# Kernel tuning notes

Measured on AMD Instinct MI355X. Metric: run time of the kernel, lower is better.

Reference implementation:

```python
import jax, jax.numpy as jnp
import numpy as np
from jax import lax

TAGSET_SIZE = 64
START_TAG = TAGSET_SIZE - 2
STOP_TAG = TAGSET_SIZE - 1
NEG_INF = -10000.0


def setup_inputs() -> dict:
    key = jax.random.key(0)
    k_feat, k_trans, k_tags = jax.random.split(key, 3)
    B, S, T = 512, 1024, TAGSET_SIZE
    feats = jax.random.normal(k_feat, (B, S, T), dtype=jnp.float32)
    transitions = jax.random.normal(k_trans, (T, T), dtype=jnp.float32)
    # CRF constraints: nothing transitions FROM anything into START row semantics
    # of the torch code: transitions[START, :] = -1e4 ; transitions[:, STOP] = -1e4
    transitions = transitions.at[START_TAG, :].set(NEG_INF)
    transitions = transitions.at[:, STOP_TAG].set(NEG_INF)
    tags = jax.random.randint(k_tags, (B, S), 0, T - 2, dtype=jnp.int64)
    mask = jnp.ones((B, S), dtype=jnp.int32)
    return {"feats": feats, "transitions": transitions, "tags": tags, "mask": mask}


def _forward_alg(feats, transitions, maskf):
    # feats: (B,S,T), maskf: (B,S) float
    B, S, T = feats.shape
    init = jnp.full((B, T), NEG_INF, dtype=feats.dtype).at[:, START_TAG].set(0.0)

    def step(fv, xs):
        feat, m = xs  # feat: (B,T), m: (B,)
        # next_tag_var[b, next, prev] = fv[b,prev] + trans[next,prev] + feat[b,next]
        nxt = jax.nn.logsumexp(
            fv[:, None, :] + transitions[None, :, :] + feat[:, :, None], axis=2
        )
        m1 = m[:, None]
        return nxt * m1 + fv * (1.0 - m1), None

    fv, _ = lax.scan(step, init, (feats.transpose(1, 0, 2), maskf.T))
    terminal = fv + transitions[STOP_TAG][None, :]
    return jax.nn.logsumexp(terminal, axis=1)  # (B,)


def _score_sentence(feats, transitions, tags, maskf):
    B, S, T = feats.shape
    tags_ext = jnp.concatenate(
        [jnp.full((B, 1), START_TAG, dtype=tags.dtype), tags], axis=1
    )  # (B, S+1)
    cur = tags_ext[:, 1:]   # (B,S)
    prev = tags_ext[:, :-1]  # (B,S)
    emit = jnp.take_along_axis(feats, cur[:, :, None], axis=2)[:, :, 0]  # (B,S)
    trans = transitions[cur, prev]  # (B,S)
    score = jnp.sum((emit + trans) * maskf, axis=1)
    last_idx = maskf.sum(axis=1).astype(jnp.int32)  # index into tags_ext
    last_tags = jnp.take_along_axis(tags_ext, last_idx[:, None].astype(tags.dtype), axis=1)[:, 0]
    return score + transitions[STOP_TAG, last_tags]


def reference(feats, transitions, tags, mask):
    maskf = mask.astype(feats.dtype)
    forward_score = _forward_alg(feats, transitions, maskf)
    gold_score = _score_sentence(feats, transitions, tags, maskf)
    return jnp.mean(forward_score - gold_score)
```

## Files before the change

kernel.cpp:

```cpp
#include <hip/hip_runtime.h>

#define START_TAG 62
#define STOP_TAG 63
#define BATCH 512
#define SLEN 1024
#define NCHAIN 64

typedef float vf4 __attribute__((ext_vector_type(4)));
typedef short short8 __attribute__((ext_vector_type(8)));

#define E_OFF_FLOATS (1u << 18)
#define E_BYTES      134217728ull
#define WS_NEEDED    (1048576ull + E_BYTES + 65536ull)

__device__ __forceinline__ unsigned pk_bf16(float lo, float hi) {
  return __builtin_amdgcn_perm(__float_as_uint(hi), __float_as_uint(lo), 0x07060302u);
}
__device__ __forceinline__ short bf16_rne(float x) {
  unsigned u = __float_as_uint(x);
  u += 0x7FFFu + ((u >> 16) & 1u);
  return (short)(u >> 16);
}
__device__ __forceinline__ vf4 mfma16(short8 a, short8 b, vf4 c) {
  return __builtin_amdgcn_mfma_f32_16x16x32_bf16(a, b, c, 0, 0, 0);
}

template<int DIR>
__device__ __forceinline__ void load_A(const float* __restrict__ trans, short8 A[4][2],
                                       int q, int col) {
  const int mrow = 16 * (col >> 2) + (col & 3);
  #pragma unroll
  for (int t = 0; t < 4; ++t) {
    #pragma unroll
    for (int c = 0; c < 2; ++c) {
      short8 a;
      #pragma unroll
      for (int j = 0; j < 8; ++j) {
        int R = mrow + 4 * t, K = 16 * q + 8 * c + j;
        float tv = (DIR == 0) ? trans[R * 64 + K] : trans[K * 64 + R];
        a[j] = bf16_rne(__expf(tv));
      }
      A[t][c] = a;
    }
  }
}

template<int DIR>
__device__ __forceinline__ void epilogue(float* __restrict__ ws, const float W[16],
                                         float C, int g, int lane, int q, int col) {
  float* slab = ws + (size_t)(g * 2 + DIR) * 1024;
  #pragma unroll
  for (int t4 = 0; t4 < 4; ++t4) {
    vf4 o = {W[t4 * 4], W[t4 * 4 + 1], W[t4 * 4 + 2], W[t4 * 4 + 3]};
    *(vf4*)(slab + lane * 16 + t4 * 4) = o;
  }
  if (q == 0) ws[65536 + (g * 2 + DIR) * 16 + col] = C;
}

template<int DIR>
__device__ __forceinline__ void crf_step(const vf4 (&Fs)[4], const short8 (&A)[4][2],
                                         float (&W)[16]) {
  float P[16];
  #pragma unroll
  for (int t = 0; t < 4; ++t)
    #pragma unroll
    for (int i = 0; i < 4; ++i)
      P[t * 4 + i] = (DIR == 0) ? W[t * 4 + i] : W[t * 4 + i] * Fs[t][i];

  union { unsigned uu[4]; short8 s8; } B0, B1;
  B0.uu[0] = pk_bf16(P[0], P[1]);   B0.uu[1] = pk_bf16(P[2], P[3]);
  B0.uu[2] = pk_bf16(P[4], P[5]);   B0.uu[3] = pk_bf16(P[6], P[7]);
  B1.uu[0] = pk_bf16(P[8], P[9]);   B1.uu[1] = pk_bf16(P[10], P[11]);
  B1.uu[2] = pk_bf16(P[12], P[13]); B1.uu[3] = pk_bf16(P[14], P[15]);

  vf4 z4 = {0.f, 0.f, 0.f, 0.f};
  vf4 d0 = mfma16(A[0][0], B0.s8, z4);
  vf4 d1 = mfma16(A[1][0], B0.s8, z4);
  vf4 d2 = mfma16(A[2][0], B0.s8, z4);
  vf4 d3 = mfma16(A[3][0], B0.s8, z4);
  d0 = mfma16(A[0][1], B1.s8, d0);
  d1 = mfma16(A[1][1], B1.s8, d1);
  d2 = mfma16(A[2][1], B1.s8, d2);
  d3 = mfma16(A[3][1], B1.s8, d3);

  #pragma unroll
  for (int i = 0; i < 4; ++i) {
    W[i]      = (DIR == 0) ? d0[i] * Fs[0][i] : d0[i];
    W[4 + i]  = (DIR == 0) ? d1[i] * Fs[1][i] : d1[i];
    W[8 + i]  = (DIR == 0) ? d2[i] * Fs[2][i] : d2[i];
    W[12 + i] = (DIR == 0) ? d3[i] * Fs[3][i] : d3[i];
  }
}

template<int DIR>
__device__ __forceinline__ void chain_fast_x(const float* E,
                                             const float* __restrict__ trans,
                                             float* __restrict__ ws, int g) {
  const int lane = threadIdx.x & 63;
  const int q = lane >> 4, col = lane & 15;

  short8 A[4][2];
  load_A<DIR>(trans, A, q, col);

  float W[16];
  if (DIR == 0) {
    #pragma unroll
    for (int i = 0; i < 16; ++i) W[i] = 0.f;
    if (q == 3) W[14] = 1.f;
  } else {
    #pragma unroll
    for (int i = 0; i < 16; ++i) W[i] = __expf(trans[STOP_TAG * 64 + 16 * q + i]);
  }

  const vf4* sp = (const vf4*)E + (((size_t)(g * 2 + DIR) * 512) << 8)
                  + (q << 4) + col;

  vf4 F[8][4];
  #pragma unroll
  for (int p = 0; p < 8; ++p)
    #pragma unroll
    for (int k = 0; k < 4; ++k)
      F[p][k] = sp[(size_t)p * 256 + k * 64];

  float C = 0.f, zpend = 1.f;

  for (int bk = 0; bk < 63; ++bk) {
    #pragma unroll
    for (int u = 0; u < 8; ++u) {
      crf_step<DIR>(F[u], A, W);
      const int jn = bk * 8 + u + 8;
      #pragma unroll
      for (int k = 0; k < 4; ++k)
        F[u][k] = sp[(size_t)jn * 256 + k * 64];
      if ((u & 3) == 3) {
        float rz = __builtin_amdgcn_rcpf(zpend);
        C += __logf(zpend);
        #pragma unroll
        for (int i = 0; i < 16; ++i) W[i] *= rz;
        zpend = __shfl(W[0], col);
      }
      __builtin_amdgcn_sched_barrier(0);
    }
  }

  #pragma unroll
  for (int u = 0; u < 8; ++u) {
    crf_step<DIR>(F[u], A, W);
    if ((u & 3) == 3) {
      float rz = __builtin_amdgcn_rcpf(zpend);
      C += __logf(zpend);
      #pragma unroll
      for (int i = 0; i < 16; ++i) W[i] *= rz;
      zpend = __shfl(W[0], col);
    }
  }

  epilogue<DIR>(ws, W, C, g, lane, q, col);
}

template<int DIR>
__device__ __forceinline__ void chain_masked(const float* __restrict__ feats,
                                             const float* __restrict__ trans,
                                             const int* __restrict__ mask,
                                             float* __restrict__ ws, int g) {
  const int lane = threadIdx.x & 63;
  const int q = lane >> 4, col = lane & 15;
  const int b = g * 16 + col;

  short8 A[4][2];
  load_A<DIR>(trans, A, q, col);

  float W[16];
  float C = 0.f;
  if (DIR == 0) {
    #pragma unroll
    for (int i = 0; i < 16; ++i) W[i] = 0.f;
    if (q == 3) W[14] = 1.f;
  } else {
    #pragma unroll
    for (int i = 0; i < 16; ++i) W[i] = __expf(trans[STOP_TAG * 64 + 16 * q + i]);
  }

  const char* gb = (const char*)feats + (size_t)b * 262144 + (size_t)q * 64;
  vf4 cur[4];
  {
    size_t s0 = (DIR == 0) ? 0 : 1023;
    #pragma unroll
    for (int v = 0; v < 4; ++v)
      cur[v] = *(const vf4*)(gb + s0 * 256 + (size_t)v * 16);
  }

  for (int grp = 0; grp < 128; ++grp) {
    #pragma unroll
    for (int u = 0; u < 4; ++u) {
      const int j = grp * 4 + u;
      float e[16];
      #pragma unroll
      for (int v = 0; v < 4; ++v)
        #pragma unroll
        for (int i = 0; i < 4; ++i) e[v * 4 + i] = __expf(cur[v][i]);

      float P[16];
      #pragma unroll
      for (int i = 0; i < 16; ++i) P[i] = (DIR == 0) ? W[i] : W[i] * e[i];

      union { unsigned uu[4]; short8 s8; } B0, B1;
      B0.uu[0] = pk_bf16(P[0], P[1]);   B0.uu[1] = pk_bf16(P[2], P[3]);
      B0.uu[2] = pk_bf16(P[4], P[5]);   B0.uu[3] = pk_bf16(P[6], P[7]);
      B1.uu[0] = pk_bf16(P[8], P[9]);   B1.uu[1] = pk_bf16(P[10], P[11]);
      B1.uu[2] = pk_bf16(P[12], P[13]); B1.uu[3] = pk_bf16(P[14], P[15]);

      vf4 z4 = {0.f, 0.f, 0.f, 0.f};
      vf4 d0 = mfma16(A[0][0], B0.s8, z4);
      vf4 d1 = mfma16(A[1][0], B0.s8, z4);
      vf4 d2 = mfma16(A[2][0], B0.s8, z4);
      vf4 d3 = mfma16(A[3][0], B0.s8, z4);
      d0 = mfma16(A[0][1], B1.s8, d0);
      d1 = mfma16(A[1][1], B1.s8, d1);
      d2 = mfma16(A[2][1], B1.s8, d2);
      d3 = mfma16(A[3][1], B1.s8, d3);

      int sj = (DIR == 0) ? j : 1023 - j;
      int m = mask[b * 1024 + sj];
      int sn = (DIR == 0) ? (j + 1) : 1023 - (j + 1);
      #pragma unroll
      for (int v = 0; v < 4; ++v)
        cur[v] = *(const vf4*)(gb + (size_t)sn * 256 + (size_t)v * 16);

      #pragma unroll
      for (int i = 0; i < 4; ++i) {
        float n0 = (DIR == 0) ? d0[i] * e[i]      : d0[i];
        float n1 = (DIR == 0) ? d1[i] * e[4 + i]  : d1[i];
        float n2 = (DIR == 0) ? d2[i] * e[8 + i]  : d2[i];
        float n3 = (DIR == 0) ? d3[i] * e[12 + i] : d3[i];
        W[i]      = m ? n0 : W[i];
        W[4 + i]  = m ? n1 : W[4 + i];
        W[8 + i]  = m ? n2 : W[8 + i];
        W[12 + i] = m ? n3 : W[12 + i];
      }
    }
    float z = __shfl(W[0], col);
    float rz = __builtin_amdgcn_rcpf(z);
    C += __logf(z);
    #pragma unroll
    for (int i = 0; i < 16; ++i) W[i] *= rz;
  }
  epilogue<DIR>(ws, W, C, g, lane, q, col);
}

__global__ __launch_bounds__(256)
void crf_prepass(const float* __restrict__ feats, float* __restrict__ E) {
  const unsigned o = blockIdx.x * 256u + threadIdx.x;
  const unsigned t    = o & 15u;
  const unsigned col  = (o >> 4) & 15u;
  const unsigned j    = (o >> 8) & 511u;
  const unsigned gd   = o >> 17;
  const unsigned dir  = gd & 1u;
  const unsigned s    = dir ? (1023u - j) : j;
  const unsigned b    = (gd >> 1) * 16u + col;

  vf4 v = ((const vf4*)feats)[(size_t)b * 16384 + (size_t)s * 16 + t];
  vf4 e;
  #pragma unroll
  for (int i = 0; i < 4; ++i) e[i] = __expf(v[i]);

  const size_t dst = (((size_t)gd * 512 + j) << 8)
                     + ((t & 3u) << 6) + ((t >> 2) << 4) + col;
  ((vf4*)E)[dst] = e;
}

template<int USE_E>
__global__ __launch_bounds__(64, 1)
void crf_main(const float* __restrict__ feats, const float* __restrict__ trans,
              const int* __restrict__ tags, const int* __restrict__ mask,
              float* __restrict__ ws, const float* E) {
  const int blk = blockIdx.x;
  if (blk < NCHAIN) {
    const int g = blk >> 1, dir = blk & 1;
    const int lane = threadIdx.x & 63;
    const int q = lane >> 4;
    const int col = lane & 15;
    const int b = g * 16 + col;
    const int sB = dir ? 512 : 0;
    int anyz = 0;
    for (int it = 0; it < 32; ++it) {
      int4 v = *(const int4*)(mask + b * 1024 + sB + (it * 4 + q) * 4);
      anyz |= (v.x == 0) | (v.y == 0) | (v.z == 0) | (v.w == 0);
    }
    bool allones = (__ballot(anyz != 0) == 0ull);
    if (USE_E && allones) {
      if (dir == 0) chain_fast_x<0>(E, trans, ws, g);
      else          chain_fast_x<1>(E, trans, ws, g);
    } else {
      if (dir == 0) chain_masked<0>(feats, trans, mask, ws, g);
      else          chain_masked<1>(feats, trans, mask, ws, g);
    }
    (void)tags;
  } else {
    const int b = blk - NCHAIN;
    const int* tb = tags + b * SLEN;
    const int* mb = mask + b * SLEN;
    const float* fbg = feats + (size_t)b * 65536;
    float acc = 0.f, cnt = 0.f;
    const int t = threadIdx.x;
    for (int k = 0; k < 16; ++k) {
      int s = t + k * 64;
      int cur = tb[s];
      int prev = (s == 0) ? START_TAG : tb[s - 1];
      float m = (float)mb[s];
      acc += m * (fbg[s * 64 + cur] + trans[cur * 64 + prev]);
      cnt += m;
    }
    #pragma unroll
    for (int o = 1; o < 64; o <<= 1) {
      acc += __shfl_xor(acc, o);
      cnt += __shfl_xor(cnt, o);
    }
    if (t == 0) {
      int last_idx = (int)(cnt + 0.5f);
      int last_tag = (last_idx == 0) ? START_TAG : tb[last_idx - 1];
      ws[66560 + b] = acc + trans[STOP_TAG * 64 + last_tag];
    }
  }
}

__global__ __launch_bounds__(512)
void crf_reduce(const float* __restrict__ ws, float* __restrict__ out) {
  __shared__ float s[512];
  const int t = threadIdx.x;
  const int g = t >> 4, col = t & 15;
  const float* Wf = ws + (size_t)(2 * g) * 1024;
  const float* Wb = ws + (size_t)(2 * g + 1) * 1024;
  float P = 0.f;
  #pragma unroll
  for (int q = 0; q < 4; ++q)
    #pragma unroll
    for (int i = 0; i < 16; ++i)
      P += Wf[(q * 16 + col) * 16 + i] * Wb[(q * 16 + col) * 16 + i];
  float sc = ws[65536 + (2 * g) * 16 + col] + ws[65536 + (2 * g + 1) * 16 + col] + __logf(P);
  s[t] = sc - ws[66560 + t];
  __syncthreads();
  for (int off = 256; off > 0; off >>= 1) {
    if (t < off) s[t] += s[t + off];
    __syncthreads();
  }
  if (t == 0) out[0] = s[0] * (1.f / 512.f);
}

extern "C" void kernel_launch(void* const* d_in, const int* in_sizes, int n_in,
                              void* d_out, int out_size, void* d_ws, size_t ws_size,
                              hipStream_t stream) {
  const float* feats = (const float*)d_in[0];
  const float* trans = (const float*)d_in[1];
  const int* tags = (const int*)d_in[2];
  const int* mask = (const int*)d_in[3];
  float* ws = (float*)d_ws;
  float* out = (float*)d_out;

  if (ws_size >= WS_NEEDED) {
    float* E = ws + E_OFF_FLOATS;
    crf_prepass<<<32768, 256, 0, stream>>>(feats, E);
    crf_main<1><<<NCHAIN + BATCH, 64, 0, stream>>>(feats, trans, tags, mask, ws, E);
  } else {
    crf_main<0><<<NCHAIN + BATCH, 64, 0, stream>>>(feats, trans, tags, mask, ws, ws);
  }
  crf_reduce<<<1, 512, 0, stream>>>(ws, out);
}
```

Baseline: 333.1 us.

## Fuse exp prepass into chain kernel with LDS producer-consumer double buffer

Drops the separate prepass kernel that exponentiated all features into a large workspace buffer. The chain kernel now runs two waves per block: one wave streams raw features into a double-buffered LDS region, and the other computes the exponentials on the fly as it runs the recurrence, with a block barrier every eight steps. This removes a full extra read and write of the feature tensor plus a kernel launch. In exchange, exp work and LDS reads now sit on the latency-bound recurrence path, and a barrier is added per chunk.

```diff
diff --git a/kernel.cpp b/kernel.cpp
--- a/kernel.cpp
+++ b/kernel.cpp
@@ -8,10 +8,6 @@
 
 typedef float vf4 __attribute__((ext_vector_type(4)));
 typedef short short8 __attribute__((ext_vector_type(8)));
-
-#define E_OFF_FLOATS (1u << 18)
-#define E_BYTES      134217728ull
-#define WS_NEEDED    (1048576ull + E_BYTES + 65536ull)
 
 __device__ __forceinline__ unsigned pk_bf16(float lo, float hi) {
   return __builtin_amdgcn_perm(__float_as_uint(hi), __float_as_uint(lo), 0x07060302u);
@@ -93,60 +89,39 @@
 }
 
 template<int DIR>
-__device__ __forceinline__ void chain_fast_x(const float* E,
-                                             const float* __restrict__ trans,
-                                             float* __restrict__ ws, int g) {
-  const int lane = threadIdx.x & 63;
+__device__ __forceinline__ void produce_chunk(const float* __restrict__ feats,
+                                              float* dst, int g, int lane, int c) {
   const int q = lane >> 4, col = lane & 15;
-
-  short8 A[4][2];
-  load_A<DIR>(trans, A, q, col);
-
-  float W[16];
-  if (DIR == 0) {
-    #pragma unroll
-    for (int i = 0; i < 16; ++i) W[i] = 0.f;
-    if (q == 3) W[14] = 1.f;
-  } else {
-    #pragma unroll
-    for (int i = 0; i < 16; ++i) W[i] = __expf(trans[STOP_TAG * 64 + 16 * q + i]);
-  }
-
-  const vf4* sp = (const vf4*)E + (((size_t)(g * 2 + DIR) * 512) << 8)
-                  + (q << 4) + col;
-
-  vf4 F[8][4];
-  #pragma unroll
-  for (int p = 0; p < 8; ++p)
-    #pragma unroll
-    for (int k = 0; k < 4; ++k)
-      F[p][k] = sp[(size_t)p * 256 + k * 64];
-
-  float C = 0.f, zpend = 1.f;
-
-  for (int bk = 0; bk < 63; ++bk) {
-    #pragma unroll
-    for (int u = 0; u < 8; ++u) {
-      crf_step<DIR>(F[u], A, W);
-      const int jn = bk * 8 + u + 8;
-      #pragma unroll
-      for (int k = 0; k < 4; ++k)
-        F[u][k] = sp[(size_t)jn * 256 + k * 64];
-      if ((u & 3) == 3) {
-        float rz = __builtin_amdgcn_rcpf(zpend);
-        C += __logf(zpend);
-        #pragma unroll
-        for (int i = 0; i < 16; ++i) W[i] *= rz;
-        zpend = __shfl(W[0], col);
-      }
-      __builtin_amdgcn_sched_barrier(0);
-    }
-  }
-
-  #pragma unroll
-  for (int u = 0; u < 8; ++u) {
-    crf_step<DIR>(F[u], A, W);
-    if ((u & 3) == 3) {
+  const int b = g * 16 + col;
+  const int jb = c * 8;
+  #pragma unroll
+  for (int st = 0; st < 8; ++st) {
+    const int j = jb + st;
+    const int s = (DIR == 0) ? j : (1023 - j);
+    const float* src = feats + (size_t)b * 65536 + (size_t)s * 64 + 16 * q;
+    #pragma unroll
+    for (int k = 0; k < 4; ++k) {
+      vf4 v = *(const vf4*)(src + 4 * k);
+      *(vf4*)(dst + st * 1024 + k * 256 + lane * 4) = v;
+    }
+  }
+}
+
+template<int DIR>
+__device__ __forceinline__ void consume_chunk(const float* buf, const short8 (&A)[4][2],
+                                              float (&W)[16], float& C, float& zpend,
+                                              int lane, int col) {
+  #pragma unroll
+  for (int st = 0; st < 8; ++st) {
+    vf4 Es[4];
+    #pragma unroll
+    for (int k = 0; k < 4; ++k) {
+      vf4 r = *(const vf4*)(buf + st * 1024 + k * 256 + lane * 4);
+      #pragma unroll
+      for (int i = 0; i < 4; ++i) Es[k][i] = __expf(r[i]);
+    }
+    crf_step<DIR>(Es, A, W);
+    if ((st & 3) == 3) {
       float rz = __builtin_amdgcn_rcpf(zpend);
       C += __logf(zpend);
       #pragma unroll
@@ -154,8 +129,48 @@
       zpend = __shfl(W[0], col);
     }
   }
-
-  epilogue<DIR>(ws, W, C, g, lane, q, col);
+}
+
+template<int DIR>
+__device__ __forceinline__ void chain_fast_pc(const float* __restrict__ feats,
+                                              const float* __restrict__ trans,
+                                              float* __restrict__ ws, int g,
+                                              float* lds) {
+  const int tid = threadIdx.x;
+  const int wid = tid >> 6;
+  const int lane = tid & 63;
+  const int q = lane >> 4, col = lane & 15;
+
+  short8 A[4][2];
+  float W[16];
+  float C = 0.f, zpend = 1.f;
+
+  if (wid == 0) {
+    load_A<DIR>(trans, A, q, col);
+    if (DIR == 0) {
+      #pragma unroll
+      for (int i = 0; i < 16; ++i) W[i] = 0.f;
+      if (q == 3) W[14] = 1.f;
+    } else {
+      #pragma unroll
+      for (int i = 0; i < 16; ++i) W[i] = __expf(trans[STOP_TAG * 64 + 16 * q + i]);
+    }
+  }
+
+  if (wid == 1) produce_chunk<DIR>(feats, lds, g, lane, 0);
+  __syncthreads();
+
+  for (int c = 0; c < 64; ++c) {
+    if (wid == 1) {
+      if (c + 1 < 64)
+        produce_chunk<DIR>(feats, lds + ((c + 1) & 1) * 8192, g, lane, c + 1);
+    } else {
+      consume_chunk<DIR>(lds + (c & 1) * 8192, A, W, C, zpend, lane, col);
+    }
+    __syncthreads();
+  }
+
+  if (wid == 0) epilogue<DIR>(ws, W, C, g, lane, q, col);
 }
 
 template<int DIR>
@@ -248,33 +263,13 @@
   epilogue<DIR>(ws, W, C, g, lane, q, col);
 }
 
-__global__ __launch_bounds__(256)
-void crf_prepass(const float* __restrict__ feats, float* __restrict__ E) {
-  const unsigned o = blockIdx.x * 256u + threadIdx.x;
-  const unsigned t    = o & 15u;
-  const unsigned col  = (o >> 4) & 15u;
-  const unsigned j    = (o >> 8) & 511u;
-  const unsigned gd   = o >> 17;
-  const unsigned dir  = gd & 1u;
-  const unsigned s    = dir ? (1023u - j) : j;
-  const unsigned b    = (gd >> 1) * 16u + col;
-
-  vf4 v = ((const vf4*)feats)[(size_t)b * 16384 + (size_t)s * 16 + t];
-  vf4 e;
-  #pragma unroll
-  for (int i = 0; i < 4; ++i) e[i] = __expf(v[i]);
-
-  const size_t dst = (((size_t)gd * 512 + j) << 8)
-                     + ((t & 3u) << 6) + ((t >> 2) << 4) + col;
-  ((vf4*)E)[dst] = e;
-}
-
-template<int USE_E>
-__global__ __launch_bounds__(64, 1)
+__global__ __launch_bounds__(128, 1)
 void crf_main(const float* __restrict__ feats, const float* __restrict__ trans,
               const int* __restrict__ tags, const int* __restrict__ mask,
-              float* __restrict__ ws, const float* E) {
+              float* __restrict__ ws) {
+  __shared__ float lds[16384];
   const int blk = blockIdx.x;
+  const int wid = threadIdx.x >> 6;
   if (blk < NCHAIN) {
     const int g = blk >> 1, dir = blk & 1;
     const int lane = threadIdx.x & 63;
@@ -288,21 +283,24 @@
       anyz |= (v.x == 0) | (v.y == 0) | (v.z == 0) | (v.w == 0);
     }
     bool allones = (__ballot(anyz != 0) == 0ull);
-    if (USE_E && allones) {
-      if (dir == 0) chain_fast_x<0>(E, trans, ws, g);
-      else          chain_fast_x<1>(E, trans, ws, g);
+    if (allones) {
+      if (dir == 0) chain_fast_pc<0>(feats, trans, ws, g, lds);
+      else          chain_fast_pc<1>(feats, trans, ws, g, lds);
     } else {
-      if (dir == 0) chain_masked<0>(feats, trans, mask, ws, g);
-      else          chain_masked<1>(feats, trans, mask, ws, g);
+      if (wid == 0) {
+        if (dir == 0) chain_masked<0>(feats, trans, mask, ws, g);
+        else          chain_masked<1>(feats, trans, mask, ws, g);
+      }
     }
     (void)tags;
   } else {
+    if (wid != 0) return;
     const int b = blk - NCHAIN;
     const int* tb = tags + b * SLEN;
     const int* mb = mask + b * SLEN;
     const float* fbg = feats + (size_t)b * 65536;
     float acc = 0.f, cnt = 0.f;
-    const int t = threadIdx.x;
+    const int t = threadIdx.x & 63;
     for (int k = 0; k < 16; ++k) {
       int s = t + k * 64;
       int cur = tb[s];
@@ -357,12 +355,6 @@
   float* ws = (float*)d_ws;
   float* out = (float*)d_out;
 
-  if (ws_size >= WS_NEEDED) {
-    float* E = ws + E_OFF_FLOATS;
-    crf_prepass<<<32768, 256, 0, stream>>>(feats, E);
-    crf_main<1><<<NCHAIN + BATCH, 64, 0, stream>>>(feats, trans, tags, mask, ws, E);
-  } else {
-    crf_main<0><<<NCHAIN + BATCH, 64, 0, stream>>>(feats, trans, tags, mask, ws, ws);
-  }
+  crf_main<<<NCHAIN + BATCH, 128, 0, stream>>>(feats, trans, tags, mask, ws);
   crf_reduce<<<1, 512, 0, stream>>>(ws, out);
 }
```

Measured after the change: 304.7 us. 8.5% less time.
